# Kernel optimization log

Hardware: AMD Instinct MI355X
Metric: run time of the kernel (lower is better)

## Reference

```python
import jax, jax.numpy as jnp
import numpy as np

PS = 8  # patch_size
EPS = 1e-5


def _layernorm(t, w, b):
    m = jnp.mean(t, axis=-1, keepdims=True)
    v = jnp.mean((t - m) ** 2, axis=-1, keepdims=True)
    return (t - m) * jax.lax.rsqrt(v + EPS) * w + b


def _to3d(t):  # B(HW)C -> BCHW
    B, N, C = t.shape
    H = W = int(np.sqrt(N))
    return t.reshape(B, H, W, C).transpose(0, 3, 1, 2)


def _to2d(t):  # BCHW -> B(HW)C
    B, C, H, W = t.shape
    return t.reshape(B, C, H * W).swapaxes(-1, -2)


def _block(t, ps=PS):  # BCHW -> [B, M, ps*ps, C] (dilated-grid blocking, as in torch code)
    B, C, H, W = t.shape
    t = t.reshape(B, C, ps, H // ps, ps, W // ps)
    t = t.transpose(0, 3, 5, 2, 4, 1)
    return t.reshape(B, (H * W) // (ps * ps), ps * ps, C)


def _unblock(t):  # inverse of _block
    B, M, N, C = t.shape
    Hb = Wb = int(np.sqrt(M))
    ps = int(np.sqrt(N))
    t = t.reshape(B, Hb, Wb, ps, ps, C)
    t = t.transpose(0, 5, 3, 1, 4, 2)
    return t.reshape(B, C, Hb * ps, Wb * ps)


def setup_inputs() -> dict:
    key = jax.random.key(0)
    ks = jax.random.split(key, 8)
    B, N, D, H = 8, 4096, 256, 8
    s = 1.0 / np.sqrt(D)
    return {
        "x": jax.random.normal(ks[0], (B, N, D), jnp.float32),
        "ln1_w": jnp.ones((D,), jnp.float32),
        "ln1_b": jnp.zeros((D,), jnp.float32),
        "q": jax.random.normal(ks[1], (H, D, D), jnp.float32) * s,
        "k": jax.random.normal(ks[2], (D, D), jnp.float32) * s,
        "v": jax.random.normal(ks[3], (D, D), jnp.float32) * s,
        "o": jax.random.normal(ks[4], (H, D, D), jnp.float32) * s,
        "ln2_w": jnp.ones((D,), jnp.float32),
        "ln2_b": jnp.zeros((D,), jnp.float32),
        "w1": jax.random.normal(ks[5], (D, D), jnp.float32) * s,
        "b1": jnp.zeros((D,), jnp.float32),
        "w2": jax.random.normal(ks[6], (D, D), jnp.float32) * s,
        "b2": jnp.zeros((D,), jnp.float32),
    }


def reference(x, ln1_w, ln1_b, q, k, v, o, ln2_w, ln2_b, w1, b1, w2, b2):
    # blocked input: [B, M, P, D], M = HW/ps^2, P = ps^2
    a = _block(_to3d(_layernorm(x, ln1_w, ln1_b)))
    nh = q.shape[0]
    Q = jnp.einsum('bmnd,hdk->bhmnk', a, q)
    Q1, Q2 = Q[:, : nh // 2], Q[:, nh // 2 :]
    K = jnp.einsum('bmnd,dk->bmnk', a, k)
    V = jnp.einsum('bmnd,dv->bmnv', a, v)
    # axis 1: attend across blocks (m) at fixed within-block position (y=n)
    s1 = jax.nn.softmax(jnp.einsum('bhxyk,bzyk->bhyxz', Q1, K), axis=-1)
    O1 = jnp.einsum('bhyxz,bzyv->bhxyv', s1, V)
    # axis 2: attend within block (n) at fixed block (x=m)
    s2 = jax.nn.softmax(jnp.einsum('bhxyk,bxzk->bhxyz', Q2, K), axis=-1)
    O2 = jnp.einsum('bhxyz,bxzv->bhxyv', s2, V)
    O = jnp.concatenate([O1, O2], axis=1)  # [B, H, M, P, D]
    # faithful to torch: 'bhmnd,hdv->bmnd' sums over h and v
    Z = jnp.einsum('bhmnd,hdv->bmnd', O, o)
    x = x + _to2d(_unblock(Z))
    h = _layernorm(x, ln2_w, ln2_b)
    mlp = jax.nn.relu(h @ w1 + b1) @ w2 + b2
    return x + mlp
```

## Files before the change

kernel.cpp:

```cpp
#include <hip/hip_runtime.h>

#define Bc   8
#define Tc   4096
#define Dc   256
#define EPSc 1e-5f

typedef _Float16 half_t;
typedef __attribute__((ext_vector_type(4))) _Float16 half4_t;
typedef __attribute__((ext_vector_type(8))) _Float16 frag8;
typedef __attribute__((ext_vector_type(4))) float f32x4;

#define MFMA_F16(a, b, c) __builtin_amdgcn_mfma_f32_16x16x32_f16((a), (b), (c), 0, 0, 0)

__global__ __launch_bounds__(256) void prep_kernel(
    const float* __restrict__ q, const float* __restrict__ k,
    const float* __restrict__ v, const float* __restrict__ w1, const float* __restrict__ w2,
    const float* __restrict__ o,
    half_t* __restrict__ Mt, half_t* vt, half_t* w1t, half_t* w2t, float* __restrict__ os) {
  __shared__ float shK[32 * 260];
  __shared__ float shQ[32 * 260];
  int bid = blockIdx.x, tid = threadIdx.x;
  if (bid < 512) {
    int h = bid >> 6, et = (bid >> 3) & 7, dt = bid & 7;
    const float* kbase = k + (size_t)(et * 32) * 256;
    const float* qbase = q + ((size_t)h * 256 + dt * 32) * 256;
    #pragma unroll
    for (int r = 0; r < 8; r++) {
      int f = r * 256 + tid;
      int row = f >> 6, c4 = (f & 63) * 4;
      *(float4*)&shK[row * 260 + c4] = *(const float4*)&kbase[(size_t)row * 256 + c4];
      *(float4*)&shQ[row * 260 + c4] = *(const float4*)&qbase[(size_t)row * 256 + c4];
    }
    __syncthreads();
    int e = tid & 31, dg = tid >> 5;
    const float* kr = &shK[e * 260];
    const float* q0 = &shQ[(dg * 4 + 0) * 260];
    const float* q1 = &shQ[(dg * 4 + 1) * 260];
    const float* q2 = &shQ[(dg * 4 + 2) * 260];
    const float* q3 = &shQ[(dg * 4 + 3) * 260];
    float a0 = 0.f, a1 = 0.f, a2 = 0.f, a3 = 0.f;
    #pragma unroll 4
    for (int kk = 0; kk < 256; kk += 4) {
      float4 kv = *(const float4*)&kr[kk];
      float4 v0 = *(const float4*)&q0[kk];
      float4 v1 = *(const float4*)&q1[kk];
      float4 v2 = *(const float4*)&q2[kk];
      float4 v3 = *(const float4*)&q3[kk];
      a0 += v0.x * kv.x + v0.y * kv.y + v0.z * kv.z + v0.w * kv.w;
      a1 += v1.x * kv.x + v1.y * kv.y + v1.z * kv.z + v1.w * kv.w;
      a2 += v2.x * kv.x + v2.y * kv.y + v2.z * kv.z + v2.w * kv.w;
      a3 += v3.x * kv.x + v3.y * kv.y + v3.z * kv.z + v3.w * kv.w;
    }
    half4_t outv;
    outv[0] = (half_t)a0; outv[1] = (half_t)a1; outv[2] = (half_t)a2; outv[3] = (half_t)a3;
    *(half4_t*)&Mt[((size_t)h * 256 + et * 32 + e) * 256 + dt * 32 + dg * 4] = outv;
  } else if (bid < 1280) {
    int b2 = bid - 512;
    int which = b2 >> 8, n = b2 & 255, d = tid;
    const float* src = which == 0 ? v : (which == 1 ? w1 : w2);
    half_t* dst = which == 0 ? vt : (which == 1 ? w1t : w2t);
    dst[(size_t)n * 256 + d] = (half_t)src[(size_t)d * 256 + n];
  } else {
    int h = bid - 1280, d = tid;
    const float* row = o + ((size_t)h * 256 + d) * 256;
    float s = 0.f;
    #pragma unroll 8
    for (int vv = 0; vv < 256; vv += 4) {
      float4 r4 = *(const float4*)&row[vv];
      s += r4.x + r4.y + r4.z + r4.w;
    }
    os[h * 256 + d] = s;
  }
}

__global__ __launch_bounds__(256, 2) void attn_kernel(
    const float* __restrict__ x, const float* __restrict__ lw, const float* __restrict__ lb,
    const half_t* __restrict__ Mt, const half_t* __restrict__ vt, const float* __restrict__ osum,
    half_t* __restrict__ Z0, half_t* __restrict__ Z1) {
  __shared__ half_t shA[64 * 264];
  __shared__ half_t shU[64 * 264 + 64 * 72];
  half_t* shVT = shU;
  half_t* shW  = shU;
  half_t* shP  = shU + 64 * 264;
  int tid = threadIdx.x, lane = tid & 63, w = tid >> 6;
  int l16 = lane & 15, quad = lane >> 4;
  int g = blockIdx.x;
  int mode = g >> 9, gg = g & 511, b = gg >> 6, slice = gg & 63;
  int hbase = mode * 4;
  half_t* Z = mode ? Z1 : Z0;

  {
    float4 wv4 = *(const float4*)&lw[lane * 4];
    float4 bv4 = *(const float4*)&lb[lane * 4];
    float4 xr[16];
    #pragma unroll
    for (int i = 0; i < 16; i++) {
      int z = w * 16 + i;
      int m = mode ? slice : z, n = mode ? z : slice;
      int hh = ((n >> 3) << 3) + (m >> 3), ww2 = ((n & 7) << 3) + (m & 7);
      int trow = b * 4096 + hh * 64 + ww2;
      xr[i] = *(const float4*)&x[(size_t)trow * 256 + lane * 4];
    }
    #pragma unroll
    for (int i = 0; i < 16; i++) {
      int z = w * 16 + i;
      float4 vv = xr[i];
      float s  = vv.x + vv.y + vv.z + vv.w;
      float sq = vv.x * vv.x + vv.y * vv.y + vv.z * vv.z + vv.w * vv.w;
      #pragma unroll
      for (int off = 1; off < 64; off <<= 1) { s += __shfl_xor(s, off); sq += __shfl_xor(sq, off); }
      float mean = s * (1.f / 256), var = sq * (1.f / 256) - mean * mean;
      float r = rsqrtf(var + EPSc);
      half4_t y;
      y[0] = (half_t)((vv.x - mean) * r * wv4.x + bv4.x);
      y[1] = (half_t)((vv.y - mean) * r * wv4.y + bv4.y);
      y[2] = (half_t)((vv.z - mean) * r * wv4.z + bv4.z);
      y[3] = (half_t)((vv.w - mean) * r * wv4.w + bv4.w);
      *(half4_t*)&shA[z * 264 + lane * 4] = y;
    }
  }
  __syncthreads();

  #pragma unroll
  for (int dth = 0; dth < 2; dth++) {
    f32x4 vacc[2][4];
    #pragma unroll
    for (int dt2 = 0; dt2 < 2; dt2++)
      #pragma unroll
      for (int zt = 0; zt < 4; zt++) vacc[dt2][zt] = (f32x4){0.f, 0.f, 0.f, 0.f};
    #pragma unroll
    for (int ks = 0; ks < 8; ks++) {
      int k0 = ks * 32 + quad * 8;
      frag8 vf0 = *(const frag8*)&vt[(size_t)(w * 64 + dth * 32 +  0 + l16) * 256 + k0];
      frag8 vf1 = *(const frag8*)&vt[(size_t)(w * 64 + dth * 32 + 16 + l16) * 256 + k0];
      frag8 bfr[4];
      #pragma unroll
      for (int zt = 0; zt < 4; zt++)
        bfr[zt] = *(const frag8*)&shA[(zt * 16 + l16) * 264 + k0];
      #pragma unroll
      for (int zt = 0; zt < 4; zt++) {
        vacc[0][zt] = MFMA_F16(vf0, bfr[zt], vacc[0][zt]);
        vacc[1][zt] = MFMA_F16(vf1, bfr[zt], vacc[1][zt]);
      }
    }
    #pragma unroll
    for (int dt2 = 0; dt2 < 2; dt2++)
      #pragma unroll
      for (int zt = 0; zt < 4; zt++)
        #pragma unroll
        for (int r = 0; r < 4; r++)
          shVT[(w * 64 + dth * 32 + dt2 * 16 + quad * 4 + r) * 72 + zt * 16 + l16] = (half_t)vacc[dt2][zt][r];
  }
  __syncthreads();

  frag8 vtreg[4][2];
  #pragma unroll
  for (int dt = 0; dt < 4; dt++)
    #pragma unroll
    for (int ks = 0; ks < 2; ks++)
      vtreg[dt][ks] = *(const frag8*)&shVT[(w * 64 + dt * 16 + l16) * 72 + ks * 32 + quad * 8];

  float osv[4][4];
  #pragma unroll
  for (int hh = 0; hh < 4; hh++)
    #pragma unroll
    for (int dt = 0; dt < 4; dt++)
      osv[hh][dt] = osum[(hbase + hh) * 256 + w * 64 + dt * 16 + l16];

  f32x4 zacc[4][4];
  #pragma unroll
  for (int mf = 0; mf < 4; mf++)
    #pragma unroll
    for (int dt = 0; dt < 4; dt++) zacc[mf][dt] = (f32x4){0.f, 0.f, 0.f, 0.f};
  __syncthreads();

  #pragma unroll
  for (int hh = 0; hh < 4; hh++) {
    const half_t* Mth = Mt + (size_t)(hbase + hh) * 65536;
    #pragma unroll
    for (int eh = 0; eh < 2; eh++) {
      f32x4 wacc[2][4];
      #pragma unroll
      for (int et2 = 0; et2 < 2; et2++)
        #pragma unroll
        for (int mf = 0; mf < 4; mf++) wacc[et2][mf] = (f32x4){0.f, 0.f, 0.f, 0.f};
      #pragma unroll
      for (int ks = 0; ks < 8; ks++) {
        int k0 = ks * 32 + quad * 8;
        frag8 bf0 = *(const frag8*)&Mth[(size_t)(w * 64 + eh * 32 +  0 + l16) * 256 + k0];
        frag8 bf1 = *(const frag8*)&Mth[(size_t)(w * 64 + eh * 32 + 16 + l16) * 256 + k0];
        frag8 af[4];
        #pragma unroll
        for (int mf = 0; mf < 4; mf++) af[mf] = *(const frag8*)&shA[(mf * 16 + l16) * 264 + k0];
        #pragma unroll
        for (int mf = 0; mf < 4; mf++) {
          wacc[0][mf] = MFMA_F16(af[mf], bf0, wacc[0][mf]);
          wacc[1][mf] = MFMA_F16(af[mf], bf1, wacc[1][mf]);
        }
      }
      #pragma unroll
      for (int et2 = 0; et2 < 2; et2++)
        #pragma unroll
        for (int mf = 0; mf < 4; mf++)
          #pragma unroll
          for (int r = 0; r < 4; r++)
            shW[(mf * 16 + quad * 4 + r) * 264 + w * 64 + eh * 32 + et2 * 16 + l16] = (half_t)wacc[et2][mf][r];
    }
    __syncthreads();
    {
      f32x4 sacc[4];
      #pragma unroll
      for (int zt = 0; zt < 4; zt++) sacc[zt] = (f32x4){0.f, 0.f, 0.f, 0.f};
      #pragma unroll
      for (int ks = 0; ks < 8; ks++) {
        int k0 = ks * 32 + quad * 8;
        frag8 wf = *(const frag8*)&shW[(w * 16 + l16) * 264 + k0];
        #pragma unroll
        for (int zt = 0; zt < 4; zt++) {
          frag8 kf = *(const frag8*)&shA[(zt * 16 + l16) * 264 + k0];
          sacc[zt] = MFMA_F16(wf, kf, sacc[zt]);
        }
      }
      #pragma unroll
      for (int r = 0; r < 4; r++) {
        float mx = fmaxf(fmaxf(sacc[0][r], sacc[1][r]), fmaxf(sacc[2][r], sacc[3][r]));
        #pragma unroll
        for (int off = 1; off < 16; off <<= 1) mx = fmaxf(mx, __shfl_xor(mx, off));
        float e0 = __expf(sacc[0][r] - mx), e1 = __expf(sacc[1][r] - mx);
        float e2 = __expf(sacc[2][r] - mx), e3 = __expf(sacc[3][r] - mx);
        float sum = e0 + e1 + e2 + e3;
        #pragma unroll
        for (int off = 1; off < 16; off <<= 1) sum += __shfl_xor(sum, off);
        float inv = 1.f / sum;
        int m = w * 16 + quad * 4 + r;
        shP[m * 72 + l16 +  0] = (half_t)(e0 * inv);
        shP[m * 72 + l16 + 16] = (half_t)(e1 * inv);
        shP[m * 72 + l16 + 32] = (half_t)(e2 * inv);
        shP[m * 72 + l16 + 48] = (half_t)(e3 * inv);
      }
    }
    __syncthreads();
    #pragma unroll
    for (int mf = 0; mf < 4; mf++) {
      frag8 pf0 = *(const frag8*)&shP[(mf * 16 + l16) * 72 +  0 + quad * 8];
      frag8 pf1 = *(const frag8*)&shP[(mf * 16 + l16) * 72 + 32 + quad * 8];
      #pragma unroll
      for (int dt = 0; dt < 4; dt++) {
        f32x4 oacc = (f32x4){0.f, 0.f, 0.f, 0.f};
        oacc = MFMA_F16(pf0, vtreg[dt][0], oacc);
        oacc = MFMA_F16(pf1, vtreg[dt][1], oacc);
        #pragma unroll
        for (int r = 0; r < 4; r++) zacc[mf][dt][r] += oacc[r] * osv[hh][dt];
      }
    }
  }

  #pragma unroll
  for (int mf = 0; mf < 4; mf++)
    #pragma unroll
    for (int dt = 0; dt < 4; dt++)
      #pragma unroll
      for (int r = 0; r < 4; r++)
        shA[(mf * 16 + quad * 4 + r) * 264 + w * 64 + dt * 16 + l16] = (half_t)zacc[mf][dt][r];
  __syncthreads();
  #pragma unroll
  for (int i = 0; i < 8; i++) {
    int slot = i * 256 + tid;
    int grow = slot >> 5, c8 = (slot & 31) * 8;
    size_t zrow = mode ? ((size_t)(b * 64 + slice) * 64 + grow) : ((size_t)(b * 64 + grow) * 64 + slice);
    *(frag8*)&Z[zrow * 256 + c8] = *(const frag8*)&shA[grow * 264 + c8];
  }
}

__global__ __launch_bounds__(256, 2) void mlp_kernel(
    const float* __restrict__ x, const half_t* __restrict__ Z0, const half_t* __restrict__ Z1,
    const float* __restrict__ lw, const float* __restrict__ lb,
    const half_t* __restrict__ w1t, const float* __restrict__ b1,
    const half_t* __restrict__ w2t, const float* __restrict__ b2,
    float* __restrict__ out) {
  __shared__ half_t shH[64 * 264];
  __shared__ half_t shHH[64 * 264];
  int tid = threadIdx.x, lane = tid & 63, w = tid >> 6;
  int l16 = lane & 15, quad = lane >> 4;
  int row0 = blockIdx.x * 64;

  #pragma unroll 4
  for (int i = 0; i < 16; i++) {
    int rl = w * 16 + i;
    int row = row0 + rl;
    size_t base = (size_t)row * 256 + lane * 4;
    int bb = row >> 12, p = row & 4095, hh = p >> 6, ww = p & 63;
    int m = (hh & 7) * 8 + (ww & 7), n = (hh >> 3) * 8 + (ww >> 3);
    size_t zbase = ((size_t)((bb * 64 + m) * 64 + n)) * 256 + lane * 4;
    float4 xv = *(const float4*)&x[base];
    half4_t zv0 = *(const half4_t*)&Z0[zbase];
    half4_t zv1 = *(const half4_t*)&Z1[zbase];
    float4 v;
    v.x = xv.x + (float)zv0[0] + (float)zv1[0];
    v.y = xv.y + (float)zv0[1] + (float)zv1[1];
    v.z = xv.z + (float)zv0[2] + (float)zv1[2];
    v.w = xv.w + (float)zv0[3] + (float)zv1[3];
    float s  = v.x + v.y + v.z + v.w;
    float sq = v.x * v.x + v.y * v.y + v.z * v.z + v.w * v.w;
    #pragma unroll
    for (int off = 1; off < 64; off <<= 1) { s += __shfl_xor(s, off); sq += __shfl_xor(sq, off); }
    float mean = s * (1.f / 256), var = sq * (1.f / 256) - mean * mean;
    float r = rsqrtf(var + EPSc);
    float4 wv = *(const float4*)&lw[lane * 4];
    float4 bv = *(const float4*)&lb[lane * 4];
    half4_t y;
    y[0] = (half_t)((v.x - mean) * r * wv.x + bv.x);
    y[1] = (half_t)((v.y - mean) * r * wv.y + bv.y);
    y[2] = (half_t)((v.z - mean) * r * wv.z + bv.z);
    y[3] = (half_t)((v.w - mean) * r * wv.w + bv.w);
    *(half4_t*)&shH[rl * 264 + lane * 4] = y;
  }
  __syncthreads();

  {
    f32x4 acc[4][4];
    #pragma unroll
    for (int mf = 0; mf < 4; mf++)
      #pragma unroll
      for (int nt = 0; nt < 4; nt++) acc[mf][nt] = (f32x4){0.f, 0.f, 0.f, 0.f};
    #pragma unroll
    for (int ks = 0; ks < 8; ks++) {
      int k0 = ks * 32 + quad * 8;
      frag8 af[4], bf[4];
      #pragma unroll
      for (int mf = 0; mf < 4; mf++) af[mf] = *(const frag8*)&shH[(mf * 16 + l16) * 264 + k0];
      #pragma unroll
      for (int nt = 0; nt < 4; nt++)
        bf[nt] = *(const frag8*)&w1t[(size_t)(w * 64 + nt * 16 + l16) * 256 + k0];
      #pragma unroll
      for (int mf = 0; mf < 4; mf++)
        #pragma unroll
        for (int nt = 0; nt < 4; nt++) acc[mf][nt] = MFMA_F16(af[mf], bf[nt], acc[mf][nt]);
    }
    #pragma unroll
    for (int mf = 0; mf < 4; mf++)
      #pragma unroll
      for (int nt = 0; nt < 4; nt++)
        #pragma unroll
        for (int r = 0; r < 4; r++) {
          int rr = mf * 16 + quad * 4 + r, col = w * 64 + nt * 16 + l16;
          float vv = acc[mf][nt][r] + b1[col];
          vv = fmaxf(vv, 0.f);
          shHH[rr * 264 + col] = (half_t)vv;
        }
  }
  __syncthreads();

  {
    f32x4 acc[4][4];
    #pragma unroll
    for (int mf = 0; mf < 4; mf++)
      #pragma unroll
      for (int nt = 0; nt < 4; nt++) acc[mf][nt] = (f32x4){0.f, 0.f, 0.f, 0.f};
    #pragma unroll
    for (int ks = 0; ks < 8; ks++) {
      int k0 = ks * 32 + quad * 8;
      frag8 af[4], bf[4];
      #pragma unroll
      for (int mf = 0; mf < 4; mf++) af[mf] = *(const frag8*)&shHH[(mf * 16 + l16) * 264 + k0];
      #pragma unroll
      for (int nt = 0; nt < 4; nt++)
        bf[nt] = *(const frag8*)&w2t[(size_t)(w * 64 + nt * 16 + l16) * 256 + k0];
      #pragma unroll
      for (int mf = 0; mf < 4; mf++)
        #pragma unroll
        for (int nt = 0; nt < 4; nt++) acc[mf][nt] = MFMA_F16(af[mf], bf[nt], acc[mf][nt]);
    }
    #pragma unroll
    for (int mf = 0; mf < 4; mf++)
      #pragma unroll
      for (int r = 0; r < 4; r++) {
        int rr = mf * 16 + quad * 4 + r;
        int row = row0 + rr;
        int bb = row >> 12, p = row & 4095, hh = p >> 6, ww = p & 63;
        int m = (hh & 7) * 8 + (ww & 7), n = (hh >> 3) * 8 + (ww >> 3);
        size_t zrow = ((size_t)((bb * 64 + m) * 64 + n)) * 256;
        size_t xrow = (size_t)row * 256;
        #pragma unroll
        for (int nt = 0; nt < 4; nt++) {
          int col = w * 64 + nt * 16 + l16;
          float vres = x[xrow + col] + (float)Z0[zrow + col] + (float)Z1[zrow + col];
          float vv = acc[mf][nt][r] + b2[col];
          out[xrow + col] = vv + vres;
        }
      }
  }
}

extern "C" void kernel_launch(void* const* d_in, const int* in_sizes, int n_in,
                              void* d_out, int out_size, void* d_ws, size_t ws_size,
                              hipStream_t stream) {
  (void)in_sizes; (void)n_in; (void)out_size; (void)ws_size;
  const float* x    = (const float*)d_in[0];
  const float* ln1w = (const float*)d_in[1];
  const float* ln1b = (const float*)d_in[2];
  const float* q    = (const float*)d_in[3];
  const float* k    = (const float*)d_in[4];
  const float* v    = (const float*)d_in[5];
  const float* o    = (const float*)d_in[6];
  const float* ln2w = (const float*)d_in[7];
  const float* ln2b = (const float*)d_in[8];
  const float* w1   = (const float*)d_in[9];
  const float* b1   = (const float*)d_in[10];
  const float* w2   = (const float*)d_in[11];
  const float* b2   = (const float*)d_in[12];
  float* out = (float*)d_out;

  const size_t ROWS = (size_t)Bc * Tc;
  const size_t ELTS = ROWS * Dc;
  const size_t MB16 = ELTS * sizeof(half_t);
  char* ws = (char*)d_ws;
  float*  osumB = (float*)ws;
  half_t* Mt    = (half_t*)(ws + (64 << 10));
  half_t* vt    = (half_t*)(ws + (64 << 10) + (1 << 20));
  half_t* w1t   = (half_t*)(ws + (64 << 10) + (1 << 20) + (128 << 10));
  half_t* w2t   = (half_t*)(ws + (64 << 10) + (1 << 20) + (256 << 10));
  half_t* Zb0   = (half_t*)(ws + (2 << 20));
  half_t* Zb1   = (half_t*)(ws + (2 << 20) + MB16);

  prep_kernel <<<1288, 256, 0, stream>>>(q, k, v, w1, w2, o, Mt, vt, w1t, w2t, osumB);
  attn_kernel <<<1024, 256, 0, stream>>>(x, ln1w, ln1b, Mt, vt, osumB, Zb0, Zb1);
  mlp_kernel  <<<ROWS / 64, 256, 0, stream>>>(x, Zb0, Zb1, ln2w, ln2b, w1t, b1, w2t, b2, out);
}
```

Baseline: 282.8 us.

## Precompute LayerNorm1 into blocked fp16 buffer in prep kernel

LayerNorm1 and the dilated-grid blocking move out of the attention kernel into extra blocks of the prep kernel. Those blocks write a half-precision, block-ordered activation buffer. Before, each row of x was normalized twice (once per attention mode) with scattered fp32 loads. Now attention blocks load contiguous fp16 rows straight into shared memory. The cost is an extra 16 MB write and read through a new workspace buffer, and a larger prep launch.

```diff
diff --git a/kernel.cpp b/kernel.cpp
--- a/kernel.cpp
+++ b/kernel.cpp
@@ -15,8 +15,10 @@
 __global__ __launch_bounds__(256) void prep_kernel(
     const float* __restrict__ q, const float* __restrict__ k,
     const float* __restrict__ v, const float* __restrict__ w1, const float* __restrict__ w2,
-    const float* __restrict__ o,
-    half_t* __restrict__ Mt, half_t* vt, half_t* w1t, half_t* w2t, float* __restrict__ os) {
+    const float* __restrict__ o, const float* __restrict__ x,
+    const float* __restrict__ lw, const float* __restrict__ lb,
+    half_t* __restrict__ Mt, half_t* vt, half_t* w1t, half_t* w2t,
+    float* __restrict__ os, half_t* __restrict__ aH) {
   __shared__ float shK[32 * 260];
   __shared__ float shQ[32 * 260];
   int bid = blockIdx.x, tid = threadIdx.x;
@@ -60,7 +62,7 @@
     const float* src = which == 0 ? v : (which == 1 ? w1 : w2);
     half_t* dst = which == 0 ? vt : (which == 1 ? w1t : w2t);
     dst[(size_t)n * 256 + d] = (half_t)src[(size_t)d * 256 + n];
-  } else {
+  } else if (bid < 1288) {
     int h = bid - 1280, d = tid;
     const float* row = o + ((size_t)h * 256 + d) * 256;
     float s = 0.f;
@@ -70,12 +72,36 @@
       s += r4.x + r4.y + r4.z + r4.w;
     }
     os[h * 256 + d] = s;
+  } else {
+    int lane = tid & 63;
+    int base_row = (bid - 1288) * 64;
+    float4 wv = *(const float4*)&lw[lane * 4];
+    float4 bv = *(const float4*)&lb[lane * 4];
+    #pragma unroll 4
+    for (int i = 0; i < 16; i++) {
+      int row = base_row + i * 4 + (tid >> 6);
+      float4 vv = *(const float4*)&x[(size_t)row * 256 + lane * 4];
+      float s  = vv.x + vv.y + vv.z + vv.w;
+      float sq = vv.x * vv.x + vv.y * vv.y + vv.z * vv.z + vv.w * vv.w;
+      #pragma unroll
+      for (int off = 1; off < 64; off <<= 1) { s += __shfl_xor(s, off); sq += __shfl_xor(sq, off); }
+      float mean = s * (1.f / 256), var = sq * (1.f / 256) - mean * mean;
+      float r = rsqrtf(var + EPSc);
+      half4_t y;
+      y[0] = (half_t)((vv.x - mean) * r * wv.x + bv.x);
+      y[1] = (half_t)((vv.y - mean) * r * wv.y + bv.y);
+      y[2] = (half_t)((vv.z - mean) * r * wv.z + bv.z);
+      y[3] = (half_t)((vv.w - mean) * r * wv.w + bv.w);
+      int bb = row >> 12, p = row & 4095, hh = p >> 6, ww = p & 63;
+      int m = (hh & 7) * 8 + (ww & 7), n = (hh >> 3) * 8 + (ww >> 3);
+      *(half4_t*)&aH[((size_t)((bb * 64 + m) * 64 + n)) * 256 + lane * 4] = y;
+    }
   }
 }
 
 __global__ __launch_bounds__(256, 2) void attn_kernel(
-    const float* __restrict__ x, const float* __restrict__ lw, const float* __restrict__ lb,
-    const half_t* __restrict__ Mt, const half_t* __restrict__ vt, const float* __restrict__ osum,
+    const half_t* __restrict__ aH, const half_t* __restrict__ Mt,
+    const half_t* __restrict__ vt, const float* __restrict__ osum,
     half_t* __restrict__ Z0, half_t* __restrict__ Z1) {
   __shared__ half_t shA[64 * 264];
   __shared__ half_t shU[64 * 264 + 64 * 72];
@@ -89,35 +115,12 @@
   int hbase = mode * 4;
   half_t* Z = mode ? Z1 : Z0;
 
-  {
-    float4 wv4 = *(const float4*)&lw[lane * 4];
-    float4 bv4 = *(const float4*)&lb[lane * 4];
-    float4 xr[16];
-    #pragma unroll
-    for (int i = 0; i < 16; i++) {
-      int z = w * 16 + i;
-      int m = mode ? slice : z, n = mode ? z : slice;
-      int hh = ((n >> 3) << 3) + (m >> 3), ww2 = ((n & 7) << 3) + (m & 7);
-      int trow = b * 4096 + hh * 64 + ww2;
-      xr[i] = *(const float4*)&x[(size_t)trow * 256 + lane * 4];
-    }
-    #pragma unroll
-    for (int i = 0; i < 16; i++) {
-      int z = w * 16 + i;
-      float4 vv = xr[i];
-      float s  = vv.x + vv.y + vv.z + vv.w;
-      float sq = vv.x * vv.x + vv.y * vv.y + vv.z * vv.z + vv.w * vv.w;
-      #pragma unroll
-      for (int off = 1; off < 64; off <<= 1) { s += __shfl_xor(s, off); sq += __shfl_xor(sq, off); }
-      float mean = s * (1.f / 256), var = sq * (1.f / 256) - mean * mean;
-      float r = rsqrtf(var + EPSc);
-      half4_t y;
-      y[0] = (half_t)((vv.x - mean) * r * wv4.x + bv4.x);
-      y[1] = (half_t)((vv.y - mean) * r * wv4.y + bv4.y);
-      y[2] = (half_t)((vv.z - mean) * r * wv4.z + bv4.z);
-      y[3] = (half_t)((vv.w - mean) * r * wv4.w + bv4.w);
-      *(half4_t*)&shA[z * 264 + lane * 4] = y;
-    }
+  #pragma unroll
+  for (int i = 0; i < 8; i++) {
+    int slot = i * 256 + tid;
+    int z = slot >> 5, c8 = (slot & 31) * 8;
+    size_t rz = mode ? ((size_t)(b * 64 + slice) * 64 + z) : ((size_t)(b * 64 + z) * 64 + slice);
+    *(frag8*)&shA[z * 264 + c8] = *(const frag8*)&aH[rz * 256 + c8];
   }
   __syncthreads();
 
@@ -420,10 +423,12 @@
   half_t* vt    = (half_t*)(ws + (64 << 10) + (1 << 20));
   half_t* w1t   = (half_t*)(ws + (64 << 10) + (1 << 20) + (128 << 10));
   half_t* w2t   = (half_t*)(ws + (64 << 10) + (1 << 20) + (256 << 10));
-  half_t* Zb0   = (half_t*)(ws + (2 << 20));
-  half_t* Zb1   = (half_t*)(ws + (2 << 20) + MB16);
-
-  prep_kernel <<<1288, 256, 0, stream>>>(q, k, v, w1, w2, o, Mt, vt, w1t, w2t, osumB);
-  attn_kernel <<<1024, 256, 0, stream>>>(x, ln1w, ln1b, Mt, vt, osumB, Zb0, Zb1);
+  half_t* aH    = (half_t*)(ws + (2 << 20));
+  half_t* Zb0   = (half_t*)(ws + (2 << 20) + MB16);
+  half_t* Zb1   = (half_t*)(ws + (2 << 20) + 2 * MB16);
+
+  prep_kernel <<<1800, 256, 0, stream>>>(q, k, v, w1, w2, o, x, ln1w, ln1b,
+                                         Mt, vt, w1t, w2t, osumB, aH);
+  attn_kernel <<<1024, 256, 0, stream>>>(aH, Mt, vt, osumB, Zb0, Zb1);
   mlp_kernel  <<<ROWS / 64, 256, 0, stream>>>(x, Zb0, Zb1, ln2w, ln2b, w1t, b1, w2t, b2, out);
 }
```

New measurement: 267.5 us (median of 4 runs). -5.4%, faster.
